# Kernel tuning notes

Measured on AMD Instinct MI355X. Metric: run time of the kernel, lower is better.

## Reference

```python
import jax, jax.numpy as jnp
import numpy as np

N_LOC, C, A, H, X, STEPS = 500000, 128, 24, 256, 128, 4


def setup_inputs() -> dict:
    key = jax.random.key(0)
    ks = jax.random.split(key, 12)
    def rn(i, shape, scale=0.05):
        return jax.random.normal(ks[i], shape, dtype=jnp.float32) * scale
    return {
        "x": jax.random.normal(ks[0], (1, X), dtype=jnp.float32),
        "h0": jnp.zeros((1, H), jnp.float32),
        "memory_contents": rn(1, (N_LOC, C), 0.01),
        "memory_addresses": rn(2, (N_LOC, A), 0.1),
        "W_query": rn(3, (H, A + C)),
        "b_query": jnp.zeros((A + C,), jnp.float32),
        "u_sharpen": rn(4, (H,)),
        "b_sharpen": jnp.zeros((1,), jnp.float32),
        "W_erase": rn(5, (H, C)),
        "b_erase": jnp.zeros((C,), jnp.float32),
        "W_cand_h": rn(6, (H, C)),
        "W_cand_x": rn(7, (X, C)),
        "b_cand": jnp.zeros((C,), jnp.float32),
        "W_ih": rn(8, (X + C, 3 * H)),
        "W_hh": rn(9, (H, 3 * H)),
        "b_ih": jnp.zeros((3 * H,), jnp.float32),
        "b_hh": jnp.zeros((3 * H,), jnp.float32),
        "num_addressing_steps": STEPS,
    }


def _gru_cell(inp, h, W_ih, W_hh, b_ih, b_hh):
    # torch.nn.GRUCell semantics
    gi = inp @ W_ih + b_ih  # (1, 3H)
    gh = h @ W_hh + b_hh    # (1, 3H)
    i_r, i_z, i_n = jnp.split(gi, 3, axis=-1)
    h_r, h_z, h_n = jnp.split(gh, 3, axis=-1)
    r = jax.nn.sigmoid(i_r + h_r)
    z = jax.nn.sigmoid(i_z + h_z)
    n = jnp.tanh(i_n + r * h_n)
    return (1.0 - z) * n + z * h


def reference(x, h0, memory_contents, memory_addresses, W_query, b_query,
              u_sharpen, b_sharpen, W_erase, b_erase, W_cand_h, W_cand_x,
              b_cand, W_ih, W_hh, b_ih, b_hh, num_addressing_steps):
    h = h0                      # (1, H)
    mem = memory_contents       # (N, C)
    for _ in range(num_addressing_steps):
        # --- content-based addressing over full memory [addresses || contents] ---
        q = h @ W_query + b_query                              # (1, A+C)
        beta = jax.nn.softplus(h @ u_sharpen + b_sharpen) + 1.0  # (1,)
        sim = memory_addresses @ q[0, :A] + mem @ q[0, A:]     # (N,)
        w = jax.nn.softmax(beta[0] * sim)                      # (N,)
        # --- read ---
        content = (w @ mem)[None, :]                           # (1, C)
        # --- controller step ---
        h = _gru_cell(jnp.concatenate([x, content], axis=1), h, W_ih, W_hh, b_ih, b_hh)
        # --- write: erase + candidate ---
        erase = jax.nn.sigmoid(h @ W_erase + b_erase)          # (1, C)
        cand = jax.nn.relu(h @ W_cand_h + x @ W_cand_x + b_cand)  # (1, C)
        mem = mem * (1.0 - w[:, None] * erase) + w[:, None] * cand
    return h
```

## Files before the change

### kernel.cpp

```cpp
#include <hip/hip_runtime.h>

#define N_LOC 500000
#define C 128
#define A 24
#define AC 152
#define H 256
#define X 128
#define G3 768
#define GRID_BIG 1024
#define MSCALE 64.0f
#define MINV 0.015625f

typedef unsigned short ushort_t;
typedef unsigned char uchar_t;
typedef float floatx2 __attribute__((ext_vector_type(2)));

__device__ __forceinline__ float sigmoidf_(float x) { return 1.0f / (1.0f + __expf(-x)); }

__device__ __forceinline__ ushort_t f2bf(float f) {
    unsigned u = __float_as_uint(f);
    u += 0x7FFFu + ((u >> 16) & 1u);
    return (ushort_t)(u >> 16);
}
__device__ __forceinline__ float bf2f(ushort_t s) {
    return __uint_as_float(((unsigned)s) << 16);
}

#if defined(__has_builtin)
#if __has_builtin(__builtin_amdgcn_cvt_pk_fp8_f32) && __has_builtin(__builtin_amdgcn_cvt_pk_f32_fp8)
#define HAVE_HW_FP8 1
#endif
#endif

__device__ __forceinline__ unsigned f2fp8_sw(float f) {
    unsigned sgn = (__float_as_uint(f) >> 24) & 0x80u;
    float af = fminf(fabsf(f), 448.0f);
    unsigned q;
    if (af < 0.015625f) {
        q = (unsigned)__float2int_rn(af * 512.0f);
    } else {
        unsigned a = __float_as_uint(af);
        a += 0x7FFFFu + ((a >> 20) & 1u);
        unsigned e = (a >> 23) - 120u;
        q = (e << 3) | ((a >> 20) & 7u);
        if (q > 126u) q = 126u;
    }
    return q | sgn;
}
__device__ __forceinline__ float fp8d_sw(unsigned b) {
    unsigned sgn = (b & 0x80u) << 24;
    unsigned e = (b >> 3) & 15u;
    unsigned m = b & 7u;
    float fn = __uint_as_float(sgn | ((e + 120u) << 23) | (m << 20));
    float fd = __uint_as_float(sgn | __float_as_uint((float)m * 0.001953125f));
    return e ? fn : fd;
}
__device__ __forceinline__ unsigned pack_fp8x4(float4 m) {
#ifdef HAVE_HW_FP8
    int w = 0;
    w = __builtin_amdgcn_cvt_pk_fp8_f32(m.x, m.y, w, false);
    w = __builtin_amdgcn_cvt_pk_fp8_f32(m.z, m.w, w, true);
    return (unsigned)w;
#else
    return f2fp8_sw(m.x) | (f2fp8_sw(m.y) << 8) | (f2fp8_sw(m.z) << 16) | (f2fp8_sw(m.w) << 24);
#endif
}
__device__ __forceinline__ float4 unpack_fp8x4(unsigned w) {
#ifdef HAVE_HW_FP8
    floatx2 lo = __builtin_amdgcn_cvt_pk_f32_fp8((int)w, false);
    floatx2 hi = __builtin_amdgcn_cvt_pk_f32_fp8((int)w, true);
    return make_float4(lo[0], lo[1], hi[0], hi[1]);
#else
    return make_float4(fp8d_sw(w & 255u), fp8d_sw((w >> 8) & 255u),
                       fp8d_sw((w >> 16) & 255u), fp8d_sw(w >> 24));
#endif
}

template <int NPREV, bool WRITE_E, bool CONVERT>
__global__ __launch_bounds__(256) void big_pass(
    const float* __restrict__ mem0, const float* __restrict__ addr,
    uchar_t* __restrict__ memq, ushort_t* __restrict__ addrbf,
    const float* __restrict__ qacc,
    const float* __restrict__ ehist,
    const float* __restrict__ chist,
    const float* __restrict__ ssum4,
    const float* __restrict__ earr,
    float* __restrict__ enew,
    float* __restrict__ part)
{
    const int lane = threadIdx.x & 31;
    const int rg   = threadIdx.x >> 5;

    float4 qc = *(const float4*)(qacc + A + 4 * lane);
    qc.x *= MINV; qc.y *= MINV; qc.z *= MINV; qc.w *= MINV;
    float4 qa = make_float4(0.f, 0.f, 0.f, 0.f);
    if (lane < 6) qa = *(const float4*)(qacc + 4 * lane);
    float beta;
    { float t = qacc[AC]; beta = (t > 20.f ? t : log1pf(__expf(t))) + 1.0f; }

    constexpr int NP = (NPREV > 0) ? NPREV : 1;
    float4 er[NP], cd[NP];
    float inv_s[NP];
#pragma unroll
    for (int s = 0; s < NPREV; ++s) {
        float4 et = *(const float4*)(ehist + (s + 1) * C + 4 * lane);
        er[s].x = sigmoidf_(et.x); er[s].y = sigmoidf_(et.y);
        er[s].z = sigmoidf_(et.z); er[s].w = sigmoidf_(et.w);
        float4 ct = *(const float4*)(chist + (s + 1) * C + 4 * lane);
        cd[s].x = fmaxf(ct.x, 0.f) * MSCALE;
        cd[s].y = fmaxf(ct.y, 0.f) * MSCALE;
        cd[s].z = fmaxf(ct.z, 0.f) * MSCALE;
        cd[s].w = fmaxf(ct.w, 0.f) * MSCALE;
        inv_s[s] = 1.0f / ssum4[s + 1];
    }

    float4 acc = make_float4(0.f, 0.f, 0.f, 0.f);
    float sumloc = 0.f;
    const int stride = gridDim.x * 8;

    for (int i = blockIdx.x * 8 + rg; i < N_LOC; i += stride) {
        float4 m, a4 = make_float4(0.f, 0.f, 0.f, 0.f);
        if (CONVERT) {
            float4 mf = *(const float4*)(mem0 + (size_t)i * C + 4 * lane);
            m.x = mf.x * MSCALE; m.y = mf.y * MSCALE;
            m.z = mf.z * MSCALE; m.w = mf.w * MSCALE;
            *(unsigned*)(memq + (size_t)i * C + 4 * lane) = pack_fp8x4(m);
            if (lane < 6) {
                a4 = *(const float4*)(addr + (size_t)i * A + 4 * lane);
                ushort4 au; au.x = f2bf(a4.x); au.y = f2bf(a4.y);
                au.z = f2bf(a4.z); au.w = f2bf(a4.w);
                *(ushort4*)(addrbf + (size_t)i * A + 4 * lane) = au;
            }
        } else {
            unsigned mw = *(const unsigned*)(memq + (size_t)i * C + 4 * lane);
            m = unpack_fp8x4(mw);
            if (lane < 6) {
                ushort4 au = *(const ushort4*)(addrbf + (size_t)i * A + 4 * lane);
                a4 = make_float4(bf2f(au.x), bf2f(au.y), bf2f(au.z), bf2f(au.w));
            }
        }

#pragma unroll
        for (int s = 0; s < NPREV; ++s) {
            float w = earr[s * N_LOC + i] * inv_s[s];
            m.x = m.x * (1.f - w * er[s].x) + w * cd[s].x;
            m.y = m.y * (1.f - w * er[s].y) + w * cd[s].y;
            m.z = m.z * (1.f - w * er[s].z) + w * cd[s].z;
            m.w = m.w * (1.f - w * er[s].w) + w * cd[s].w;
        }

        float sv = m.x * qc.x + m.y * qc.y + m.z * qc.z + m.w * qc.w;
        sv += a4.x * qa.x + a4.y * qa.y + a4.z * qa.z + a4.w * qa.w;
        sv += __shfl_xor(sv, 1);
        sv += __shfl_xor(sv, 2);
        sv += __shfl_xor(sv, 4);
        sv += __shfl_xor(sv, 8);
        sv += __shfl_xor(sv, 16);
        float ev = __expf(beta * sv);
        if (WRITE_E && lane == 0) enew[i] = ev;
        if (lane == 0) sumloc += ev;
        acc.x += ev * m.x; acc.y += ev * m.y;
        acc.z += ev * m.z; acc.w += ev * m.w;
    }

    __shared__ float sc[8][C];
    __shared__ float ssum[256];
    *(float4*)(&sc[rg][4 * lane]) = acc;
    ssum[threadIdx.x] = sumloc;
    __syncthreads();
    if (threadIdx.x < C) {
        float v = 0.f;
#pragma unroll
        for (int g = 0; g < 8; ++g) v += sc[g][threadIdx.x];
        part[(size_t)threadIdx.x * GRID_BIG + blockIdx.x] = v;
    }
    for (int off = 128; off > 0; off >>= 1) {
        if (threadIdx.x < off) ssum[threadIdx.x] += ssum[threadIdx.x + off];
        __syncthreads();
    }
    if (threadIdx.x == 0) part[(size_t)C * GRID_BIG + blockIdx.x] = ssum[0];
}

__global__ __launch_bounds__(256) void reduce_part(
    const float* __restrict__ part, float* __restrict__ craw,
    float* __restrict__ ssum4, int step)
{
    const int j = blockIdx.x;
    float v = 0.f;
    for (int b = threadIdx.x; b < GRID_BIG; b += 256)
        v += part[(size_t)j * GRID_BIG + b];
    __shared__ float sh[256];
    sh[threadIdx.x] = v;
    __syncthreads();
    for (int off = 128; off > 0; off >>= 1) {
        if (threadIdx.x < off) sh[threadIdx.x] += sh[threadIdx.x + off];
        __syncthreads();
    }
    if (threadIdx.x == 0) {
        craw[j] = sh[0];
        if (j == C) ssum4[step] = sh[0];
    }
}

__global__ __launch_bounds__(256) void prex(
    const float* __restrict__ x, const float* __restrict__ W_ih,
    const float* __restrict__ b_ih, const float* __restrict__ W_cx,
    float* __restrict__ gix, float* __restrict__ candx)
{
    const int tid = threadIdx.x;
    float a0 = 0.f, a1 = 0.f, a2 = 0.f, ac = 0.f;
    const int k0 = blockIdx.x * 8;
    for (int k = k0; k < k0 + 8; ++k) {
        float xk = x[k];
        const float* row = W_ih + (size_t)k * G3;
        a0 += xk * row[tid];
        a1 += xk * row[256 + tid];
        a2 += xk * row[512 + tid];
        if (tid < C) ac += xk * W_cx[k * C + tid];
    }
    const bool b0 = (blockIdx.x == 0);
    atomicAdd(gix + tid,        a0 + (b0 ? b_ih[tid] : 0.f));
    atomicAdd(gix + 256 + tid,  a1 + (b0 ? b_ih[256 + tid] : 0.f));
    atomicAdd(gix + 512 + tid,  a2 + (b0 ? b_ih[512 + tid] : 0.f));
    if (tid < C) atomicAdd(candx + tid, ac);
}

__global__ __launch_bounds__(256) void post(
    const float* __restrict__ h,
    const float* __restrict__ W_er, const float* __restrict__ b_er,
    const float* __restrict__ W_ch, const float* __restrict__ b_cd,
    const float* __restrict__ W_q,  const float* __restrict__ b_q,
    const float* __restrict__ u_sh, const float* __restrict__ b_sh,
    const float* __restrict__ candx,
    float* __restrict__ eslot, float* __restrict__ cslot,
    float* __restrict__ qacc)
{
    const int tid = threadIdx.x;
    float ae = 0.f, ac = 0.f, aq = 0.f, ab = 0.f;
    const int k0 = blockIdx.x * 16;
    for (int k = k0; k < k0 + 16; ++k) {
        float hk = h[k];
        if (tid < C)  { ae += hk * W_er[k * C + tid]; ac += hk * W_ch[k * C + tid]; }
        if (tid < AC)   aq += hk * W_q[k * AC + tid];
        if (tid == 255) ab += hk * u_sh[k];
    }
    const bool b0 = (blockIdx.x == 0);
    if (tid < C) {
        atomicAdd(eslot + tid, ae + (b0 ? b_er[tid] : 0.f));
        atomicAdd(cslot + tid, ac + (b0 ? (candx[tid] + b_cd[tid]) : 0.f));
    }
    if (tid < AC)   atomicAdd(qacc + tid, aq + (b0 ? b_q[tid] : 0.f));
    if (tid == 255) atomicAdd(qacc + AC, ab + (b0 ? b_sh[0] : 0.f));
}

__global__ __launch_bounds__(256) void gatesfin(
    const float* __restrict__ craw, const float* __restrict__ hprev,
    const float* __restrict__ W_ih, const float* __restrict__ W_hh,
    const float* __restrict__ b_hh, const float* __restrict__ gix,
    float* __restrict__ p2, float* __restrict__ hout,
    float* __restrict__ qacc, unsigned* __restrict__ counter)
{
    const int tid = threadIdx.x;
    const float inv = MINV / craw[C];
    float gi0 = 0.f, gi1 = 0.f, gi2 = 0.f, gh0 = 0.f, gh1 = 0.f, gh2 = 0.f;
    const int kc0 = blockIdx.x * 8;
    for (int k = kc0; k < kc0 + 8; ++k) {
        float ck = craw[k] * inv;
        const float* row = W_ih + (size_t)(X + k) * G3;
        gi0 += ck * row[tid]; gi1 += ck * row[256 + tid]; gi2 += ck * row[512 + tid];
    }
    const int kh0 = blockIdx.x * 16;
    for (int k = kh0; k < kh0 + 16; ++k) {
        float hk = hprev[k];
        const float* row = W_hh + (size_t)k * G3;
        gh0 += hk * row[tid]; gh1 += hk * row[256 + tid]; gh2 += hk * row[512 + tid];
    }
    const bool b0 = (blockIdx.x == 0);
    float* pb = p2 + blockIdx.x * 1536;
    pb[tid]        = gi0 + (b0 ? gix[tid] : 0.f);
    pb[256 + tid]  = gi1 + (b0 ? gix[256 + tid] : 0.f);
    pb[512 + tid]  = gi2 + (b0 ? gix[512 + tid] : 0.f);
    pb[768 + tid]  = gh0 + (b0 ? b_hh[tid] : 0.f);
    pb[1024 + tid] = gh1 + (b0 ? b_hh[256 + tid] : 0.f);
    pb[1280 + tid] = gh2 + (b0 ? b_hh[512 + tid] : 0.f);
    __threadfence();
    __syncthreads();
    __shared__ int lastBlk;
    if (tid == 0) lastBlk = (atomicAdd(counter, 1u) == 15u) ? 1 : 0;
    __syncthreads();
    if (!lastBlk) return;
    __threadfence();
    float ir = 0.f, iz = 0.f, in_ = 0.f, hr = 0.f, hz = 0.f, hn = 0.f;
    for (int b = 0; b < 16; ++b) {
        const float* q = p2 + b * 1536;
        ir += q[tid]; iz += q[256 + tid]; in_ += q[512 + tid];
        hr += q[768 + tid]; hz += q[1024 + tid]; hn += q[1280 + tid];
    }
    float r = sigmoidf_(ir + hr);
    float z = sigmoidf_(iz + hz);
    float n = tanhf(in_ + r * hn);
    hout[tid] = (1.f - z) * n + z * hprev[tid];
    if (tid < 160) qacc[tid] = 0.f;
    if (tid == 0) *counter = 0u;
}

extern "C" void kernel_launch(void* const* d_in, const int* in_sizes, int n_in,
                              void* d_out, int out_size, void* d_ws, size_t ws_size,
                              hipStream_t stream) {
    (void)in_sizes; (void)n_in; (void)out_size; (void)ws_size;
    const float* x    = (const float*)d_in[0];
    const float* h0   = (const float*)d_in[1];
    const float* mem0 = (const float*)d_in[2];
    const float* addr = (const float*)d_in[3];
    const float* W_q  = (const float*)d_in[4];
    const float* b_q  = (const float*)d_in[5];
    const float* u_sh = (const float*)d_in[6];
    const float* b_sh = (const float*)d_in[7];
    const float* W_er = (const float*)d_in[8];
    const float* b_er = (const float*)d_in[9];
    const float* W_ch = (const float*)d_in[10];
    const float* W_cx = (const float*)d_in[11];
    const float* b_cd = (const float*)d_in[12];
    const float* W_ih = (const float*)d_in[13];
    const float* W_hh = (const float*)d_in[14];
    const float* b_ih = (const float*)d_in[15];
    const float* b_hh = (const float*)d_in[16];
    float* hout = (float*)d_out;

    float*    e      = (float*)d_ws;
    uchar_t*  memq   = (uchar_t*)(e + 3 * N_LOC);
    ushort_t* addrbf = (ushort_t*)(memq + (size_t)N_LOC * C);
    float*    part   = (float*)(addrbf + (size_t)N_LOC * A);
    float*    S      = part + 132 * GRID_BIG;
    float*    craw   = S;
    float*    qacc   = S + 144;
    float*    ehist  = S + 304;
    float*    chist  = S + 816;
    float*    gix    = S + 1328;
    float*    candx  = S + 2096;
    float*    ssum4  = S + 2224;
    unsigned* counter= (unsigned*)(S + 2232);
    float*    p2     = S + 2240;

    hipMemsetAsync(S, 0, 2240 * sizeof(float), stream);
    prex<<<16, 256, 0, stream>>>(x, W_ih, b_ih, W_cx, gix, candx);
    post<<<16, 256, 0, stream>>>(h0, W_er, b_er, W_ch, b_cd, W_q, b_q, u_sh, b_sh,
                                 candx, ehist, chist, qacc);
    big_pass<0, true, true><<<GRID_BIG, 256, 0, stream>>>(
        mem0, addr, memq, addrbf, qacc, ehist, chist, ssum4, e, e, part);
    reduce_part<<<129, 256, 0, stream>>>(part, craw, ssum4, 1);
    gatesfin<<<16, 256, 0, stream>>>(craw, h0, W_ih, W_hh, b_hh, gix, p2, hout,
                                     qacc, counter);
    post<<<16, 256, 0, stream>>>(hout, W_er, b_er, W_ch, b_cd, W_q, b_q, u_sh, b_sh,
                                 candx, ehist + C, chist + C, qacc);
    big_pass<1, true, false><<<GRID_BIG, 256, 0, stream>>>(
        mem0, addr, memq, addrbf, qacc, ehist, chist, ssum4, e, e + N_LOC, part);
    reduce_part<<<129, 256, 0, stream>>>(part, craw, ssum4, 2);
    gatesfin<<<16, 256, 0, stream>>>(craw, hout, W_ih, W_hh, b_hh, gix, p2, hout,
                                     qacc, counter);
    post<<<16, 256, 0, stream>>>(hout, W_er, b_er, W_ch, b_cd, W_q, b_q, u_sh, b_sh,
                                 candx, ehist + 2 * C, chist + 2 * C, qacc);
    big_pass<2, true, false><<<GRID_BIG, 256, 0, stream>>>(
        mem0, addr, memq, addrbf, qacc, ehist, chist, ssum4, e, e + 2 * N_LOC, part);
    reduce_part<<<129, 256, 0, stream>>>(part, craw, ssum4, 3);
    gatesfin<<<16, 256, 0, stream>>>(craw, hout, W_ih, W_hh, b_hh, gix, p2, hout,
                                     qacc, counter);
    post<<<16, 256, 0, stream>>>(hout, W_er, b_er, W_ch, b_cd, W_q, b_q, u_sh, b_sh,
                                 candx, ehist + 3 * C, chist + 3 * C, qacc);
    big_pass<3, false, false><<<GRID_BIG, 256, 0, stream>>>(
        mem0, addr, memq, addrbf, qacc, ehist, chist, ssum4, e, e, part);
    reduce_part<<<129, 256, 0, stream>>>(part, craw, ssum4, 4);
    gatesfin<<<16, 256, 0, stream>>>(craw, hout, W_ih, W_hh, b_hh, gix, p2, hout,
                                     qacc, counter);
}
```

Baseline: 736.5 us.

## Fuse all addressing steps into one cooperative persistent kernel with grid syncs

Measured after the change: 2.605 ms. 3.54x slower.

```diff
diff --git a/kernel.cpp b/kernel.cpp
--- a/kernel.cpp
+++ b/kernel.cpp
@@ -1,4 +1,7 @@
 #include <hip/hip_runtime.h>
+#include <hip/hip_cooperative_groups.h>
+
+namespace cg = cooperative_groups;
 
 #define N_LOC 500000
 #define C 128
@@ -76,20 +79,33 @@
 #endif
 }
 
+struct Params {
+    const float *x, *h0, *mem0, *addr;
+    const float *W_q, *b_q, *u_sh, *b_sh, *W_er, *b_er, *W_ch, *W_cx, *b_cd;
+    const float *W_ih, *W_hh, *b_ih, *b_hh;
+    float *hout;
+    float *e;
+    uchar_t *memq;
+    ushort_t *addrbf;
+    float *craw;
+    float *qacc;
+    float *ehist;
+    float *chist;
+    float *gix;
+    float *candx;
+    float *ssum4;
+    float *gacc;
+    float *hbuf;
+    unsigned *counter;
+};
+
 template <int NPREV, bool WRITE_E, bool CONVERT>
-__global__ __launch_bounds__(256) void big_pass(
-    const float* __restrict__ mem0, const float* __restrict__ addr,
-    uchar_t* __restrict__ memq, ushort_t* __restrict__ addrbf,
-    const float* __restrict__ qacc,
-    const float* __restrict__ ehist,
-    const float* __restrict__ chist,
-    const float* __restrict__ ssum4,
-    const float* __restrict__ earr,
-    float* __restrict__ enew,
-    float* __restrict__ part)
+__device__ void big_body(const Params& P, float* __restrict__ enew,
+                         float (*sc)[C], float* ssum)
 {
     const int lane = threadIdx.x & 31;
     const int rg   = threadIdx.x >> 5;
+    const float* qacc = P.qacc;
 
     float4 qc = *(const float4*)(qacc + A + 4 * lane);
     qc.x *= MINV; qc.y *= MINV; qc.z *= MINV; qc.w *= MINV;
@@ -98,6 +114,246 @@
     float beta;
     { float t = qacc[AC]; beta = (t > 20.f ? t : log1pf(__expf(t))) + 1.0f; }
 
+    constexpr int NP = (NPREV > 0) ? NPREV : 1;
+    float4 er[NP], cd[NP];
+    float inv_s[NP];
+#pragma unroll
+    for (int s = 0; s < NPREV; ++s) {
+        float4 et = *(const float4*)(P.ehist + (s + 1) * C + 4 * lane);
+        er[s].x = sigmoidf_(et.x); er[s].y = sigmoidf_(et.y);
+        er[s].z = sigmoidf_(et.z); er[s].w = sigmoidf_(et.w);
+        float4 ct = *(const float4*)(P.chist + (s + 1) * C + 4 * lane);
+        cd[s].x = fmaxf(ct.x, 0.f) * MSCALE;
+        cd[s].y = fmaxf(ct.y, 0.f) * MSCALE;
+        cd[s].z = fmaxf(ct.z, 0.f) * MSCALE;
+        cd[s].w = fmaxf(ct.w, 0.f) * MSCALE;
+        inv_s[s] = 1.0f / P.ssum4[s + 1];
+    }
+
+    float4 acc = make_float4(0.f, 0.f, 0.f, 0.f);
+    float sumloc = 0.f;
+    const int stride = GRID_BIG * 8;
+
+    for (int i = blockIdx.x * 8 + rg; i < N_LOC; i += stride) {
+        float4 m, a4 = make_float4(0.f, 0.f, 0.f, 0.f);
+        if (CONVERT) {
+            float4 mf = *(const float4*)(P.mem0 + (size_t)i * C + 4 * lane);
+            m.x = mf.x * MSCALE; m.y = mf.y * MSCALE;
+            m.z = mf.z * MSCALE; m.w = mf.w * MSCALE;
+            *(unsigned*)(P.memq + (size_t)i * C + 4 * lane) = pack_fp8x4(m);
+            if (lane < 6) {
+                a4 = *(const float4*)(P.addr + (size_t)i * A + 4 * lane);
+                ushort4 au; au.x = f2bf(a4.x); au.y = f2bf(a4.y);
+                au.z = f2bf(a4.z); au.w = f2bf(a4.w);
+                *(ushort4*)(P.addrbf + (size_t)i * A + 4 * lane) = au;
+            }
+        } else {
+            unsigned mw = *(const unsigned*)(P.memq + (size_t)i * C + 4 * lane);
+            m = unpack_fp8x4(mw);
+            if (lane < 6) {
+                ushort4 au = *(const ushort4*)(P.addrbf + (size_t)i * A + 4 * lane);
+                a4 = make_float4(bf2f(au.x), bf2f(au.y), bf2f(au.z), bf2f(au.w));
+            }
+        }
+
+#pragma unroll
+        for (int s = 0; s < NPREV; ++s) {
+            float w = P.e[s * N_LOC + i] * inv_s[s];
+            m.x = m.x * (1.f - w * er[s].x) + w * cd[s].x;
+            m.y = m.y * (1.f - w * er[s].y) + w * cd[s].y;
+            m.z = m.z * (1.f - w * er[s].z) + w * cd[s].z;
+            m.w = m.w * (1.f - w * er[s].w) + w * cd[s].w;
+        }
+
+        float sv = m.x * qc.x + m.y * qc.y + m.z * qc.z + m.w * qc.w;
+        sv += a4.x * qa.x + a4.y * qa.y + a4.z * qa.z + a4.w * qa.w;
+        sv += __shfl_xor(sv, 1);
+        sv += __shfl_xor(sv, 2);
+        sv += __shfl_xor(sv, 4);
+        sv += __shfl_xor(sv, 8);
+        sv += __shfl_xor(sv, 16);
+        float ev = __expf(beta * sv);
+        if (WRITE_E && lane == 0) enew[i] = ev;
+        if (lane == 0) sumloc += ev;
+        acc.x += ev * m.x; acc.y += ev * m.y;
+        acc.z += ev * m.z; acc.w += ev * m.w;
+    }
+
+    *(float4*)(&sc[rg][4 * lane]) = acc;
+    ssum[threadIdx.x] = sumloc;
+    __syncthreads();
+    if (threadIdx.x < C) {
+        float v = 0.f;
+#pragma unroll
+        for (int g = 0; g < 8; ++g) v += sc[g][threadIdx.x];
+        atomicAdd(P.craw + threadIdx.x, v);
+    }
+    for (int off = 128; off > 0; off >>= 1) {
+        if (threadIdx.x < off) ssum[threadIdx.x] += ssum[threadIdx.x + off];
+        __syncthreads();
+    }
+    if (threadIdx.x == 0) atomicAdd(P.craw + C, ssum[0]);
+}
+
+__device__ void proj_phase(const Params& P, const float* __restrict__ h,
+                           float* __restrict__ eslot, float* __restrict__ cslot,
+                           bool doEC, bool addQBias)
+{
+    const int tid = threadIdx.x;
+    const int bid = blockIdx.x;
+    const int k0 = bid * 2;
+    const float hv0 = h[k0], hv1 = h[k0 + 1];
+    if (tid < AC) {
+        float a = hv0 * P.W_q[k0 * AC + tid] + hv1 * P.W_q[(k0 + 1) * AC + tid];
+        if (addQBias && bid == 0) a += P.b_q[tid];
+        atomicAdd(P.qacc + tid, a);
+    } else if (tid == AC) {
+        float a = hv0 * P.u_sh[k0] + hv1 * P.u_sh[k0 + 1];
+        if (addQBias && bid == 0) a += P.b_sh[0];
+        atomicAdd(P.qacc + AC, a);
+    }
+    if (doEC && tid < C) {
+        float ev = hv0 * P.W_er[k0 * C + tid] + hv1 * P.W_er[(k0 + 1) * C + tid];
+        float cv = hv0 * P.W_ch[k0 * C + tid] + hv1 * P.W_ch[(k0 + 1) * C + tid];
+        atomicAdd(eslot + tid, ev);
+        atomicAdd(cslot + tid, cv);
+    }
+}
+
+__device__ void prex_phase(const Params& P, int pb)
+{
+    const int tid = threadIdx.x;
+    const int k0 = pb * 2;
+    const float x0 = P.x[k0], x1 = P.x[k0 + 1];
+    const float* r0 = P.W_ih + (size_t)k0 * G3;
+    const float* r1 = P.W_ih + (size_t)(k0 + 1) * G3;
+    float g0 = x0 * r0[tid]       + x1 * r1[tid];
+    float g1 = x0 * r0[256 + tid] + x1 * r1[256 + tid];
+    float g2 = x0 * r0[512 + tid] + x1 * r1[512 + tid];
+    if (pb == 0) { g0 += P.b_ih[tid]; g1 += P.b_ih[256 + tid]; g2 += P.b_ih[512 + tid]; }
+    atomicAdd(P.gix + tid, g0);
+    atomicAdd(P.gix + 256 + tid, g1);
+    atomicAdd(P.gix + 512 + tid, g2);
+    if (tid < C)
+        atomicAdd(P.candx + tid, x0 * P.W_cx[k0 * C + tid] + x1 * P.W_cx[(k0 + 1) * C + tid]);
+}
+
+__device__ void gates_phase(const Params& P, const float* __restrict__ hprev, int step)
+{
+    const int tid = threadIdx.x;
+    const int bid = blockIdx.x;
+    if (bid < 96) {
+        if (bid < 32) {
+            const float inv = MINV / P.craw[C];
+            float g0 = 0.f, g1 = 0.f, g2 = 0.f;
+            const int k0 = bid * 4;
+            for (int k = k0; k < k0 + 4; ++k) {
+                float ck = P.craw[k] * inv;
+                const float* row = P.W_ih + (size_t)(X + k) * G3;
+                g0 += ck * row[tid]; g1 += ck * row[256 + tid]; g2 += ck * row[512 + tid];
+            }
+            atomicAdd(P.gacc + tid, g0);
+            atomicAdd(P.gacc + 256 + tid, g1);
+            atomicAdd(P.gacc + 512 + tid, g2);
+        } else {
+            float g0 = 0.f, g1 = 0.f, g2 = 0.f;
+            const int k0 = (bid - 32) * 4;
+            for (int k = k0; k < k0 + 4; ++k) {
+                float hk = hprev[k];
+                const float* row = P.W_hh + (size_t)k * G3;
+                g0 += hk * row[tid]; g1 += hk * row[256 + tid]; g2 += hk * row[512 + tid];
+            }
+            atomicAdd(P.gacc + 768 + tid, g0);
+            atomicAdd(P.gacc + 1024 + tid, g1);
+            atomicAdd(P.gacc + 1280 + tid, g2);
+        }
+        __threadfence();
+        __syncthreads();
+        __shared__ int lastBlk;
+        if (tid == 0) lastBlk = (atomicAdd(P.counter, 1u) == 95u) ? 1 : 0;
+        __syncthreads();
+        if (lastBlk) {
+            __threadfence();
+            float ir  = P.gacc[tid]        + P.gix[tid];
+            float iz  = P.gacc[256 + tid]  + P.gix[256 + tid];
+            float in_ = P.gacc[512 + tid]  + P.gix[512 + tid];
+            float hr  = P.gacc[768 + tid]  + P.b_hh[tid];
+            float hz  = P.gacc[1024 + tid] + P.b_hh[256 + tid];
+            float hn  = P.gacc[1280 + tid] + P.b_hh[512 + tid];
+            float r = sigmoidf_(ir + hr);
+            float z = sigmoidf_(iz + hz);
+            float n = tanhf(in_ + r * hn);
+            float h = (1.f - z) * n + z * hprev[tid];
+            if (step == 4) P.hout[tid] = h; else P.hbuf[tid] = h;
+            if (tid == 0) P.ssum4[step] = P.craw[C];
+            if (step < 4) {
+                if (tid < AC)       P.qacc[tid] = P.b_q[tid];
+                else if (tid == AC) P.qacc[AC]  = P.b_sh[0];
+                else if (tid < 160) P.qacc[tid] = 0.f;
+                if (tid < C) {
+                    P.ehist[step * C + tid] = P.b_er[tid];
+                    P.chist[step * C + tid] = P.candx[tid] + P.b_cd[tid];
+                }
+                if (tid < 132) P.craw[tid] = 0.f;
+                for (int j = tid; j < 1536; j += 256) P.gacc[j] = 0.f;
+                if (tid == 0) *P.counter = 0u;
+            }
+            __threadfence();
+        }
+    }
+}
+
+__global__ void __launch_bounds__(256, 4) mega(Params P)
+{
+    cg::grid_group grid = cg::this_grid();
+    __shared__ float sc[8][C];
+    __shared__ float ssum[256];
+    const int bid = blockIdx.x;
+
+    if (bid < 128)       proj_phase(P, P.h0, nullptr, nullptr, false, true);
+    else if (bid < 192)  prex_phase(P, bid - 128);
+    __threadfence(); grid.sync();
+
+    big_body<0, true, true>(P, P.e, sc, ssum);
+    __threadfence(); grid.sync();
+    gates_phase(P, P.h0, 1);
+    __threadfence(); grid.sync();
+    if (bid < 128) proj_phase(P, P.hbuf, P.ehist + 1 * C, P.chist + 1 * C, true, false);
+    __threadfence(); grid.sync();
+    big_body<1, true, false>(P, P.e + N_LOC, sc, ssum);
+    __threadfence(); grid.sync();
+    gates_phase(P, P.hbuf, 2);
+    __threadfence(); grid.sync();
+    if (bid < 128) proj_phase(P, P.hbuf, P.ehist + 2 * C, P.chist + 2 * C, true, false);
+    __threadfence(); grid.sync();
+    big_body<2, true, false>(P, P.e + 2 * N_LOC, sc, ssum);
+    __threadfence(); grid.sync();
+    gates_phase(P, P.hbuf, 3);
+    __threadfence(); grid.sync();
+    if (bid < 128) proj_phase(P, P.hbuf, P.ehist + 3 * C, P.chist + 3 * C, true, false);
+    __threadfence(); grid.sync();
+    big_body<3, false, false>(P, P.e, sc, ssum);
+    __threadfence(); grid.sync();
+    gates_phase(P, P.hbuf, 4);
+}
+
+template <int NPREV, bool WRITE_E, bool CONVERT>
+__global__ __launch_bounds__(256) void big_pass_fb(
+    const float* __restrict__ mem0, const float* __restrict__ addr,
+    uchar_t* __restrict__ memq, ushort_t* __restrict__ addrbf,
+    const float* __restrict__ qacc, const float* __restrict__ ehist,
+    const float* __restrict__ chist, const float* __restrict__ ssum4,
+    const float* __restrict__ earr, float* __restrict__ enew,
+    float* __restrict__ part)
+{
+    const int lane = threadIdx.x & 31;
+    const int rg   = threadIdx.x >> 5;
+    float4 qc = *(const float4*)(qacc + A + 4 * lane);
+    qc.x *= MINV; qc.y *= MINV; qc.z *= MINV; qc.w *= MINV;
+    float4 qa = make_float4(0.f, 0.f, 0.f, 0.f);
+    if (lane < 6) qa = *(const float4*)(qacc + 4 * lane);
+    float beta;
+    { float t = qacc[AC]; beta = (t > 20.f ? t : log1pf(__expf(t))) + 1.0f; }
     constexpr int NP = (NPREV > 0) ? NPREV : 1;
     float4 er[NP], cd[NP];
     float inv_s[NP];
@@ -107,17 +363,13 @@
         er[s].x = sigmoidf_(et.x); er[s].y = sigmoidf_(et.y);
         er[s].z = sigmoidf_(et.z); er[s].w = sigmoidf_(et.w);
         float4 ct = *(const float4*)(chist + (s + 1) * C + 4 * lane);
-        cd[s].x = fmaxf(ct.x, 0.f) * MSCALE;
-        cd[s].y = fmaxf(ct.y, 0.f) * MSCALE;
-        cd[s].z = fmaxf(ct.z, 0.f) * MSCALE;
-        cd[s].w = fmaxf(ct.w, 0.f) * MSCALE;
+        cd[s].x = fmaxf(ct.x, 0.f) * MSCALE; cd[s].y = fmaxf(ct.y, 0.f) * MSCALE;
+        cd[s].z = fmaxf(ct.z, 0.f) * MSCALE; cd[s].w = fmaxf(ct.w, 0.f) * MSCALE;
         inv_s[s] = 1.0f / ssum4[s + 1];
     }
-
     float4 acc = make_float4(0.f, 0.f, 0.f, 0.f);
     float sumloc = 0.f;
     const int stride = gridDim.x * 8;
-
     for (int i = blockIdx.x * 8 + rg; i < N_LOC; i += stride) {
         float4 m, a4 = make_float4(0.f, 0.f, 0.f, 0.f);
         if (CONVERT) {
@@ -139,7 +391,6 @@
                 a4 = make_float4(bf2f(au.x), bf2f(au.y), bf2f(au.z), bf2f(au.w));
             }
         }
-
 #pragma unroll
         for (int s = 0; s < NPREV; ++s) {
             float w = earr[s * N_LOC + i] * inv_s[s];
@@ -148,21 +399,16 @@
             m.z = m.z * (1.f - w * er[s].z) + w * cd[s].z;
             m.w = m.w * (1.f - w * er[s].w) + w * cd[s].w;
         }
-
         float sv = m.x * qc.x + m.y * qc.y + m.z * qc.z + m.w * qc.w;
         sv += a4.x * qa.x + a4.y * qa.y + a4.z * qa.z + a4.w * qa.w;
-        sv += __shfl_xor(sv, 1);
-        sv += __shfl_xor(sv, 2);
-        sv += __shfl_xor(sv, 4);
-        sv += __shfl_xor(sv, 8);
-        sv += __shfl_xor(sv, 16);
+        sv += __shfl_xor(sv, 1); sv += __shfl_xor(sv, 2); sv += __shfl_xor(sv, 4);
+        sv += __shfl_xor(sv, 8); sv += __shfl_xor(sv, 16);
         float ev = __expf(beta * sv);
         if (WRITE_E && lane == 0) enew[i] = ev;
         if (lane == 0) sumloc += ev;
         acc.x += ev * m.x; acc.y += ev * m.y;
         acc.z += ev * m.z; acc.w += ev * m.w;
     }
-
     __shared__ float sc[8][C];
     __shared__ float ssum[256];
     *(float4*)(&sc[rg][4 * lane]) = acc;
@@ -213,15 +459,13 @@
     for (int k = k0; k < k0 + 8; ++k) {
         float xk = x[k];
         const float* row = W_ih + (size_t)k * G3;
-        a0 += xk * row[tid];
-        a1 += xk * row[256 + tid];
-        a2 += xk * row[512 + tid];
+        a0 += xk * row[tid]; a1 += xk * row[256 + tid]; a2 += xk * row[512 + tid];
         if (tid < C) ac += xk * W_cx[k * C + tid];
     }
     const bool b0 = (blockIdx.x == 0);
-    atomicAdd(gix + tid,        a0 + (b0 ? b_ih[tid] : 0.f));
-    atomicAdd(gix + 256 + tid,  a1 + (b0 ? b_ih[256 + tid] : 0.f));
-    atomicAdd(gix + 512 + tid,  a2 + (b0 ? b_ih[512 + tid] : 0.f));
+    atomicAdd(gix + tid,       a0 + (b0 ? b_ih[tid] : 0.f));
+    atomicAdd(gix + 256 + tid, a1 + (b0 ? b_ih[256 + tid] : 0.f));
+    atomicAdd(gix + 512 + tid, a2 + (b0 ? b_ih[512 + tid] : 0.f));
     if (tid < C) atomicAdd(candx + tid, ac);
 }
 
@@ -330,46 +574,65 @@
     float*    e      = (float*)d_ws;
     uchar_t*  memq   = (uchar_t*)(e + 3 * N_LOC);
     ushort_t* addrbf = (ushort_t*)(memq + (size_t)N_LOC * C);
-    float*    part   = (float*)(addrbf + (size_t)N_LOC * A);
-    float*    S      = part + 132 * GRID_BIG;
+    float*    S      = (float*)(addrbf + (size_t)N_LOC * A);
     float*    craw   = S;
     float*    qacc   = S + 144;
     float*    ehist  = S + 304;
-    float*    chist  = S + 816;
-    float*    gix    = S + 1328;
-    float*    candx  = S + 2096;
-    float*    ssum4  = S + 2224;
-    unsigned* counter= (unsigned*)(S + 2232);
-    float*    p2     = S + 2240;
-
-    hipMemsetAsync(S, 0, 2240 * sizeof(float), stream);
-    prex<<<16, 256, 0, stream>>>(x, W_ih, b_ih, W_cx, gix, candx);
-    post<<<16, 256, 0, stream>>>(h0, W_er, b_er, W_ch, b_cd, W_q, b_q, u_sh, b_sh,
-                                 candx, ehist, chist, qacc);
-    big_pass<0, true, true><<<GRID_BIG, 256, 0, stream>>>(
-        mem0, addr, memq, addrbf, qacc, ehist, chist, ssum4, e, e, part);
-    reduce_part<<<129, 256, 0, stream>>>(part, craw, ssum4, 1);
-    gatesfin<<<16, 256, 0, stream>>>(craw, h0, W_ih, W_hh, b_hh, gix, p2, hout,
-                                     qacc, counter);
-    post<<<16, 256, 0, stream>>>(hout, W_er, b_er, W_ch, b_cd, W_q, b_q, u_sh, b_sh,
-                                 candx, ehist + C, chist + C, qacc);
-    big_pass<1, true, false><<<GRID_BIG, 256, 0, stream>>>(
-        mem0, addr, memq, addrbf, qacc, ehist, chist, ssum4, e, e + N_LOC, part);
-    reduce_part<<<129, 256, 0, stream>>>(part, craw, ssum4, 2);
-    gatesfin<<<16, 256, 0, stream>>>(craw, hout, W_ih, W_hh, b_hh, gix, p2, hout,
-                                     qacc, counter);
-    post<<<16, 256, 0, stream>>>(hout, W_er, b_er, W_ch, b_cd, W_q, b_q, u_sh, b_sh,
-                                 candx, ehist + 2 * C, chist + 2 * C, qacc);
-    big_pass<2, true, false><<<GRID_BIG, 256, 0, stream>>>(
-        mem0, addr, memq, addrbf, qacc, ehist, chist, ssum4, e, e + 2 * N_LOC, part);
-    reduce_part<<<129, 256, 0, stream>>>(part, craw, ssum4, 3);
-    gatesfin<<<16, 256, 0, stream>>>(craw, hout, W_ih, W_hh, b_hh, gix, p2, hout,
-                                     qacc, counter);
-    post<<<16, 256, 0, stream>>>(hout, W_er, b_er, W_ch, b_cd, W_q, b_q, u_sh, b_sh,
-                                 candx, ehist + 3 * C, chist + 3 * C, qacc);
-    big_pass<3, false, false><<<GRID_BIG, 256, 0, stream>>>(
-        mem0, addr, memq, addrbf, qacc, ehist, chist, ssum4, e, e, part);
-    reduce_part<<<129, 256, 0, stream>>>(part, craw, ssum4, 4);
-    gatesfin<<<16, 256, 0, stream>>>(craw, hout, W_ih, W_hh, b_hh, gix, p2, hout,
-                                     qacc, counter);
-}
+    float*    chist  = S + 944;
+    float*    gix    = S + 1584;
+    float*    candx  = S + 2352;
+    float*    ssum4  = S + 2480;
+    unsigned* counter= (unsigned*)(S + 2488);
+    float*    gacc   = S + 2496;
+    float*    hbuf   = S + 4032;
+    float*    part   = S + 4352;
+    float*    p2     = part + 132 * GRID_BIG;
+
+    hipMemsetAsync(S, 0, 4288 * sizeof(float), stream);
+
+    Params Pr;
+    Pr.x = x; Pr.h0 = h0; Pr.mem0 = mem0; Pr.addr = addr;
+    Pr.W_q = W_q; Pr.b_q = b_q; Pr.u_sh = u_sh; Pr.b_sh = b_sh;
+    Pr.W_er = W_er; Pr.b_er = b_er; Pr.W_ch = W_ch; Pr.W_cx = W_cx; Pr.b_cd = b_cd;
+    Pr.W_ih = W_ih; Pr.W_hh = W_hh; Pr.b_ih = b_ih; Pr.b_hh = b_hh;
+    Pr.hout = hout; Pr.e = e; Pr.memq = memq; Pr.addrbf = addrbf;
+    Pr.craw = craw; Pr.qacc = qacc; Pr.ehist = ehist; Pr.chist = chist;
+    Pr.gix = gix; Pr.candx = candx; Pr.ssum4 = ssum4; Pr.gacc = gacc;
+    Pr.hbuf = hbuf; Pr.counter = counter;
+
+    void* kargs[] = { (void*)&Pr };
+    hipError_t ce = hipLaunchCooperativeKernel((const void*)mega, dim3(GRID_BIG),
+                                               dim3(256), kargs, 0, stream);
+    if (ce != hipSuccess) {
+        (void)hipGetLastError();
+        prex<<<16, 256, 0, stream>>>(x, W_ih, b_ih, W_cx, gix, candx);
+        post<<<16, 256, 0, stream>>>(h0, W_er, b_er, W_ch, b_cd, W_q, b_q, u_sh, b_sh,
+                                     candx, ehist, chist, qacc);
+        big_pass_fb<0, true, true><<<GRID_BIG, 256, 0, stream>>>(
+            mem0, addr, memq, addrbf, qacc, ehist, chist, ssum4, e, e, part);
+        reduce_part<<<129, 256, 0, stream>>>(part, craw, ssum4, 1);
+        gatesfin<<<16, 256, 0, stream>>>(craw, h0, W_ih, W_hh, b_hh, gix, p2, hout,
+                                         qacc, counter);
+        post<<<16, 256, 0, stream>>>(hout, W_er, b_er, W_ch, b_cd, W_q, b_q, u_sh, b_sh,
+                                     candx, ehist + C, chist + C, qacc);
+        big_pass_fb<1, true, false><<<GRID_BIG, 256, 0, stream>>>(
+            mem0, addr, memq, addrbf, qacc, ehist, chist, ssum4, e, e + N_LOC, part);
+        reduce_part<<<129, 256, 0, stream>>>(part, craw, ssum4, 2);
+        gatesfin<<<16, 256, 0, stream>>>(craw, hout, W_ih, W_hh, b_hh, gix, p2, hout,
+                                         qacc, counter);
+        post<<<16, 256, 0, stream>>>(hout, W_er, b_er, W_ch, b_cd, W_q, b_q, u_sh, b_sh,
+                                     candx, ehist + 2 * C, chist + 2 * C, qacc);
+        big_pass_fb<2, true, false><<<GRID_BIG, 256, 0, stream>>>(
+            mem0, addr, memq, addrbf, qacc, ehist, chist, ssum4, e, e + 2 * N_LOC, part);
+        reduce_part<<<129, 256, 0, stream>>>(part, craw, ssum4, 3);
+        gatesfin<<<16, 256, 0, stream>>>(craw, hout, W_ih, W_hh, b_hh, gix, p2, hout,
+                                         qacc, counter);
+        post<<<16, 256, 0, stream>>>(hout, W_er, b_er, W_ch, b_cd, W_q, b_q, u_sh, b_sh,
+                                     candx, ehist + 3 * C, chist + 3 * C, qacc);
+        big_pass_fb<3, false, false><<<GRID_BIG, 256, 0, stream>>>(
+            mem0, addr, memq, addrbf, qacc, ehist, chist, ssum4, e, e, part);
+        reduce_part<<<129, 256, 0, stream>>>(part, craw, ssum4, 4);
+        gatesfin<<<16, 256, 0, stream>>>(craw, hout, W_ih, W_hh, b_hh, gix, p2, hout,
+                                         qacc, counter);
+    }
+}
```
